# Performance work log

Hardware: AMD Instinct MI355X
Metric: run time of the kernel (lower is better)

## Reference

```python
import jax, jax.numpy as jnp
import numpy as np

L = 512      # number of residues
Q = 21       # alphabet size (20 AAs + gap)
N = 4096     # number of sequences
RES = 400    # residue_idx: number of already-known sites (< L)
BETA = 1.0   # inverse temperature


def setup_inputs() -> dict:
    key = jax.random.key(0)
    k_tok, k_h, k_J = jax.random.split(key, 3)
    # One-hot encoded partial MSA: [N, RES, Q]
    tokens = jax.random.randint(k_tok, (N, RES), 0, Q)
    X = jax.nn.one_hot(tokens, Q, dtype=jnp.float32)
    # Learned parameters (init scale 1e-4 as in the torch module)
    h = jax.random.normal(k_h, (L, Q), dtype=jnp.float32) * 1e-4
    J = jax.random.normal(k_J, (L, Q, L, Q), dtype=jnp.float32) * 1e-4
    return {"X": X, "h": h, "J": J}


def reference(X, h, J):
    # residue_idx = X.shape[1] (static under jit)
    n_samples, i, q = X.shape
    # J[i, :, :i, :] -> [q, i*q]; X -> [n, i*q]
    J_ar = J[i, :, :i, :].reshape(q, i * q)
    logit_i = h[i] + jnp.einsum('ij,nj->ni', J_ar, X.reshape(n_samples, i * q))
    return jax.nn.softmax(BETA * logit_i, axis=-1)  # [n, q]
```

## Files before the change

### kernel.cpp

```cpp
#include <hip/hip_runtime.h>


#define QA    21
#define RESI  400
#define NSEQ  4096
#define NT    6
#define NBX   683
#define SJ    16
#define NST   25
#define STAGE_F  (NT*SJ*QA)
#define STAGE_V4 (STAGE_F/4)
#define JQ2_ELEMS (RESI*QA*QA)

#define GLOAD_LDS16(g, l)                                                     \
    __builtin_amdgcn_global_load_lds(                                         \
        (const __attribute__((address_space(1))) void*)(g),                   \
        (__attribute__((address_space(3))) void*)(l), 16, 0, 0)

__global__ __launch_bounds__(256) void k0_jq2(const float* __restrict__ J,
                                              float* __restrict__ Jq2) {
    int s = blockIdx.x * 256 + threadIdx.x;
    if (s >= JQ2_ELEMS) return;
    int q  = s / 8400;
    int ja = s - q * 8400;
    Jq2[ja * 21 + q] = J[(8400 + q) * 10752 + ja];
}

__global__ __launch_bounds__(128) void k1_main(const float* __restrict__ X,
                                               const float* __restrict__ Jq2,
                                               const float* __restrict__ h,
                                               float* __restrict__ out) {
    __shared__ float buf[2][STAGE_F];
    __shared__ int   tokb[2][NT * SJ];
    __shared__ float lg[NT * QA];

    const int tid = threadIdx.x;
    const int n0  = blockIdx.x * NT;

    const int w    = tid >> 6, l = tid & 63;
    const int q    = l % 21;
    const int ns   = l / 21;
    const int nloc = w * 3 + ns;
    const bool act = (l < 63);

    auto issue = [&](int s) {
        const int jb = s * SJ;
        float* dst = &buf[s & 1][0];
        #pragma unroll
        for (int k = 0; k < 4; ++k) {
            int e = tid + (k << 7);
            if (e < STAGE_V4) {
                int row = e / 84;
                int col = e - row * 84;
                int nr  = n0 + row;
                if (nr >= NSEQ) nr = n0;
                const float* gp = X + (nr * RESI + jb) * QA + (col << 2);
                GLOAD_LDS16(gp, dst + (e << 2));
            }
        }
    };

    float acc = 0.f;
    issue(0);

    for (int s = 0; s < NST; ++s) {
        const int p = s & 1;
        if (s + 1 < NST) {
            issue(s + 1);
            asm volatile("s_waitcnt vmcnt(4)" ::: "memory");
        } else {
            asm volatile("s_waitcnt vmcnt(0)" ::: "memory");
        }
        __builtin_amdgcn_s_barrier();
        __builtin_amdgcn_sched_barrier(0);

        if (tid < NT * SJ) {
            const int r = tid >> 4, jj = tid & 15;
            const float* cell = &buf[p][r * (SJ * QA) + jj * QA];
            float fa = 0.f;
            #pragma unroll
            for (int a = 0; a < QA; ++a) fa = fmaf(cell[a], (float)a, fa);
            tokb[p][tid] = (int)(fa + 0.5f);
        }
        asm volatile("s_waitcnt lgkmcnt(0)" ::: "memory");
        __builtin_amdgcn_s_barrier();
        __builtin_amdgcn_sched_barrier(0);

        if (act) {
            const int jb441 = s * (SJ * 441);
            const int4* tp = (const int4*)&tokb[p][nloc * SJ];
            #pragma unroll
            for (int g = 0; g < 4; ++g) {
                int4 t4 = tp[g];
                acc += Jq2[jb441 + (4 * g + 0) * 441 + t4.x * 21 + q];
                acc += Jq2[jb441 + (4 * g + 1) * 441 + t4.y * 21 + q];
                acc += Jq2[jb441 + (4 * g + 2) * 441 + t4.z * 21 + q];
                acc += Jq2[jb441 + (4 * g + 3) * 441 + t4.w * 21 + q];
            }
        }
    }

    if (act) lg[nloc * QA + q] = acc + h[8400 + q];
    __syncthreads();
    if (tid < NT * QA) {
        const int nl = tid / QA, q2 = tid - nl * QA;
        const int n  = n0 + nl;
        if (n < NSEQ) {
            const float* rowp = lg + nl * QA;
            float m = -1e30f;
            #pragma unroll
            for (int a = 0; a < QA; ++a) m = fmaxf(m, rowp[a]);
            float den = 0.f;
            #pragma unroll
            for (int a = 0; a < QA; ++a) den += __expf(rowp[a] - m);
            out[n * QA + q2] = __expf(rowp[q2] - m) / den;
        }
    }
}

extern "C" void kernel_launch(void* const* d_in, const int* in_sizes, int n_in,
                              void* d_out, int out_size, void* d_ws, size_t ws_size,
                              hipStream_t stream) {
    const float* X = (const float*)d_in[0];
    const float* h = (const float*)d_in[1];
    const float* J = (const float*)d_in[2];
    float* out = (float*)d_out;

    float* Jq2 = (float*)d_ws;

    k0_jq2<<<(JQ2_ELEMS + 255) / 256, 256, 0, stream>>>(J, Jq2);
    k1_main<<<NBX, 128, 0, stream>>>(X, Jq2, h, out);
}
```

Before: 44.35 us.

## Split residue range across waves with cross-wave reduction and larger stages

Each block now handles 3 sequences with 256 threads. The four waves each take a quarter of every 40-residue stage and combine their partial logits through shared memory before the softmax. Stage count drops from 25 to 10, global source pointers are precomputed once, and the grid doubles to 1366 blocks. The aim is more parallelism per sequence, fewer barrier round trips and less address arithmetic, at the cost of an extra reduction step, larger LDS stages and possibly lower occupancy.

```diff
diff --git a/kernel.cpp b/kernel.cpp
--- a/kernel.cpp
+++ b/kernel.cpp
@@ -1,15 +1,15 @@
 #include <hip/hip_runtime.h>
 
 
-#define QA    21
-#define RESI  400
-#define NSEQ  4096
-#define NT    6
-#define NBX   683
-#define SJ    16
-#define NST   25
-#define STAGE_F  (NT*SJ*QA)
+#define QA      21
+#define RESI    400
+#define NSEQ    4096
+#define ROWS    3
+#define SJ      40
+#define NST     10
+#define STAGE_F (ROWS*SJ*QA)
 #define STAGE_V4 (STAGE_F/4)
+#define NBX     1366
 #define JQ2_ELEMS (RESI*QA*QA)
 
 #define GLOAD_LDS16(g, l)                                                     \
@@ -26,57 +26,62 @@
     Jq2[ja * 21 + q] = J[(8400 + q) * 10752 + ja];
 }
 
-__global__ __launch_bounds__(128) void k1_main(const float* __restrict__ X,
+__global__ __launch_bounds__(256) void k1_main(const float* __restrict__ X,
                                                const float* __restrict__ Jq2,
                                                const float* __restrict__ h,
                                                float* __restrict__ out) {
     __shared__ float buf[2][STAGE_F];
-    __shared__ int   tokb[2][NT * SJ];
-    __shared__ float lg[NT * QA];
+    __shared__ int   tokb[2][ROWS * SJ];
+    __shared__ float comb[4][63];
+    __shared__ float lg[63];
 
     const int tid = threadIdx.x;
-    const int n0  = blockIdx.x * NT;
+    const int w   = tid >> 6, l = tid & 63;
+    const int n0  = blockIdx.x * ROWS;
 
-    const int w    = tid >> 6, l = tid & 63;
-    const int q    = l % 21;
-    const int ns   = l / 21;
-    const int nloc = w * 3 + ns;
+    const char* Xb = (const char*)X;
+    const char* pbase[3];
+    bool pv[3];
+    #pragma unroll
+    for (int k = 0; k < 3; ++k) {
+        int e   = tid + (k << 8);
+        pv[k]   = (e < STAGE_V4);
+        int row = e / 210;
+        int col = e - row * 210;
+        int nr  = n0 + row; if (nr > NSEQ - 1) nr = NSEQ - 1;
+        pbase[k] = Xb + (size_t)nr * 33600 + (size_t)col * 16;
+    }
+
+    const int  q   = l % 21;
+    const int  ns  = l / 21;
     const bool act = (l < 63);
 
     auto issue = [&](int s) {
-        const int jb = s * SJ;
-        float* dst = &buf[s & 1][0];
+        char* dst = (char*)&buf[s & 1][0];
         #pragma unroll
-        for (int k = 0; k < 4; ++k) {
-            int e = tid + (k << 7);
-            if (e < STAGE_V4) {
-                int row = e / 84;
-                int col = e - row * 84;
-                int nr  = n0 + row;
-                if (nr >= NSEQ) nr = n0;
-                const float* gp = X + (nr * RESI + jb) * QA + (col << 2);
-                GLOAD_LDS16(gp, dst + (e << 2));
-            }
-        }
+        for (int k = 0; k < 3; ++k)
+            if (pv[k])
+                GLOAD_LDS16(pbase[k] + s * 3360, dst + ((tid + (k << 8)) << 4));
     };
 
+    issue(0);
     float acc = 0.f;
-    issue(0);
 
+    #pragma unroll 2
     for (int s = 0; s < NST; ++s) {
         const int p = s & 1;
         if (s + 1 < NST) {
             issue(s + 1);
-            asm volatile("s_waitcnt vmcnt(4)" ::: "memory");
+            if (w < 2) asm volatile("s_waitcnt vmcnt(3)" ::: "memory");
+            else       asm volatile("s_waitcnt vmcnt(2)" ::: "memory");
         } else {
             asm volatile("s_waitcnt vmcnt(0)" ::: "memory");
         }
         __builtin_amdgcn_s_barrier();
         __builtin_amdgcn_sched_barrier(0);
 
-        if (tid < NT * SJ) {
-            const int r = tid >> 4, jj = tid & 15;
-            const float* cell = &buf[p][r * (SJ * QA) + jj * QA];
+        if (tid < ROWS * SJ) {
+            const float* cell = &buf[p][tid * QA];
             float fa = 0.f;
             #pragma unroll
             for (int a = 0; a < QA; ++a) fa = fmaf(cell[a], (float)a, fa);
@@ -87,33 +92,33 @@
         __builtin_amdgcn_sched_barrier(0);
 
         if (act) {
-            const int jb441 = s * (SJ * 441);
-            const int4* tp = (const int4*)&tokb[p][nloc * SJ];
+            const int jb = s * SJ + w * 10;
+            const int* tp = &tokb[p][ns * SJ + w * 10];
             #pragma unroll
-            for (int g = 0; g < 4; ++g) {
-                int4 t4 = tp[g];
-                acc += Jq2[jb441 + (4 * g + 0) * 441 + t4.x * 21 + q];
-                acc += Jq2[jb441 + (4 * g + 1) * 441 + t4.y * 21 + q];
-                acc += Jq2[jb441 + (4 * g + 2) * 441 + t4.z * 21 + q];
-                acc += Jq2[jb441 + (4 * g + 3) * 441 + t4.w * 21 + q];
+            for (int jj = 0; jj < 10; ++jj) {
+                int t = tp[jj];
+                acc += Jq2[(jb + jj) * 441 + t * 21 + q];
             }
         }
     }
 
-    if (act) lg[nloc * QA + q] = acc + h[8400 + q];
+    if (act) comb[w][l] = acc;
     __syncthreads();
-    if (tid < NT * QA) {
-        const int nl = tid / QA, q2 = tid - nl * QA;
-        const int n  = n0 + nl;
-        if (n < NSEQ) {
-            const float* rowp = lg + nl * QA;
+    if (tid < 63)
+        lg[tid] = comb[0][tid] + comb[1][tid] + comb[2][tid] + comb[3][tid]
+                + h[8400 + tid % 21];
+    __syncthreads();
+    if (tid < 63) {
+        const int nn = n0 + ns;
+        if (nn < NSEQ) {
+            const float* r = lg + ns * 21;
             float m = -1e30f;
             #pragma unroll
-            for (int a = 0; a < QA; ++a) m = fmaxf(m, rowp[a]);
+            for (int a = 0; a < QA; ++a) m = fmaxf(m, r[a]);
             float den = 0.f;
             #pragma unroll
-            for (int a = 0; a < QA; ++a) den += __expf(rowp[a] - m);
-            out[n * QA + q2] = __expf(rowp[q2] - m) / den;
+            for (int a = 0; a < QA; ++a) den += __expf(r[a] - m);
+            out[nn * QA + q] = __expf(r[q] - m) / den;
         }
     }
 }
@@ -129,5 +134,5 @@
     float* Jq2 = (float*)d_ws;
 
     k0_jq2<<<(JQ2_ELEMS + 255) / 256, 256, 0, stream>>>(J, Jq2);
-    k1_main<<<NBX, 128, 0, stream>>>(X, Jq2, h, out);
+    k1_main<<<NBX, 256, 0, stream>>>(X, Jq2, h, out);
 }
```

New measurement: 40.76 us. -8.1%, faster.
